# Optimization experiments

Hardware: AMD Instinct MI355X
Metric: run time of the kernel (lower is better)

## Reference

```python
import jax, jax.numpy as jnp
import numpy as np

N_DATASETS = 2
DATASET_CATS = (1536, 1536)
TOTAL_CATS = 3072
MAX_UNIFY = 1536
N_NODES = TOTAL_CATS + MAX_UNIFY  # 4608
LRELU_ALPHA = 0.2
BI_TEMP = 0.05
NEG_INF = -9e15


def setup_inputs() -> dict:
    key = jax.random.key(0)
    ks = jax.random.split(key, 12)
    nfeat, nfeat_out, nfeat_adj, nhid, nheads = 512, 256, 64, 64, 4
    att_out, mlp = 256, 512
    s = lambda k, sh: (jax.random.normal(k, sh, jnp.float32) * 0.05)
    return {
        'x': jax.random.normal(ks[0], (N_NODES, nfeat), jnp.float32),
        'W_before': s(ks[1], (nfeat, nfeat_out)),
        'b_before': jnp.zeros((nfeat_out,), jnp.float32),
        'W_adj': s(ks[2], (nfeat_out, nfeat_adj)),
        'b_adj': jnp.zeros((nfeat_adj,), jnp.float32),
        'W_heads': s(ks[3], (nheads, nfeat_out, nhid)),
        'a_heads': s(ks[4], (nheads, 2 * nhid)),
        'W_out': s(ks[5], (nheads * nhid, att_out)),
        'a_out': s(ks[6], (2 * att_out,)),
        'W_lin1': s(ks[7], (att_out, mlp)),
        'b_lin1': jnp.zeros((mlp,), jnp.float32),
    }


def _calc_adjacency(x_out, W_adj, b_adj):
    # linear_adj + L2 normalize + cosine similarity + row normalization via diag(1/rowsum)
    af = x_out @ W_adj + b_adj                              # [N, nfeat_adj]
    nrm = jnp.sqrt(jnp.sum(af * af, axis=1, keepdims=True))
    naf = af / jnp.maximum(nrm, 1e-12)
    sim = naf @ naf.T                                       # [N, N]
    rowsum = jnp.sum(sim, axis=1)
    r_inv = 1.0 / rowsum
    r_inv = jnp.where(jnp.isinf(r_inv), 0.0, r_inv)
    return r_inv[:, None] * sim                             # diag(1/rowsum) @ sim


def _gat_multihead(x, adj, W, a):
    # W: [H, F, d], a: [H, 2d]. Standard pyGAT dense attention, vectorized over heads.
    d = W.shape[-1]
    Wh = jnp.einsum('nf,hfd->hnd', x, W)                    # [H, N, d]
    f1 = jnp.einsum('hnd,hd->hn', Wh, a[:, :d])             # [H, N]
    f2 = jnp.einsum('hnd,hd->hn', Wh, a[:, d:])             # [H, N]
    e = jax.nn.leaky_relu(f1[:, :, None] + f2[:, None, :], LRELU_ALPHA)  # [H, N, N]
    att = jnp.where(adj[None] > 0, e, NEG_INF)
    att = jax.nn.softmax(att, axis=-1)
    return jnp.einsum('hnm,hmd->hnd', att, Wh)              # [H, N, d]


def _gat_single(x, adj, W, a):
    d = W.shape[-1]
    Wh = x @ W                                              # [N, d]
    f1 = Wh @ a[:d]
    f2 = Wh @ a[d:]
    e = jax.nn.leaky_relu(f1[:, None] + f2[None, :], LRELU_ALPHA)
    att = jnp.where(adj > 0, e, NEG_INF)
    att = jax.nn.softmax(att, axis=-1)
    return att @ Wh


def reference(x, W_before, b_before, W_adj, b_adj, W_heads, a_heads, W_out, a_out, W_lin1, b_lin1):
    x1 = x @ W_before + b_before                            # linear_before
    adj = _calc_adjacency(x1, W_adj, b_adj)                 # before relu, as in source
    x1 = jax.nn.relu(x1)
    # multi-head GAT layer 1 (concat=True -> elu per head, concat along feature dim)
    h = jax.nn.elu(_gat_multihead(x1, adj, W_heads, a_heads))   # [H, N, d]
    H, N, d = h.shape
    feat = jnp.transpose(h, (1, 0, 2)).reshape(N, H * d)
    x2 = feat + x1                                          # residual; dropout is eval no-op
    # output attention head (concat=False -> no elu inside)
    x3 = jax.nn.elu(_gat_single(x2, adj, W_out, a_out) + x2)
    feat_mlp = x3 @ W_lin1 + b_lin1                          # linear1
    # sep_bipartite_graphs: per-dataset column-softmax over unify columns
    bgs = []
    cur = 0
    for nc in DATASET_CATS:
        blk = adj[cur:cur + nc, TOTAL_CATS:]                 # [nc, MAX_UNIFY]
        bgs.append(jax.nn.softmax(blk / BI_TEMP, axis=0))
        cur += nc
    return (feat_mlp[TOTAL_CATS:],) + tuple(bgs)


if __name__ == '__main__':
    out = reference(**setup_inputs())
    for o in out:
        print(o.shape, o.dtype)
```

## Files before the change

### kernel.cpp

```cpp
#include <hip/hip_runtime.h>
#include <hip/hip_bf16.h>
#include <math.h>

constexpr int NTOT = 4608;
constexpr int TC   = 3072;
constexpr int MU   = 1536;
constexpr int NH   = 4;

constexpr long OFF_ADJ  = 0;
constexpr long OFF_X1   = OFF_ADJ  + (long)NTOT*NTOT;
constexpr long OFF_NAF  = OFF_X1   + (long)NTOT*256;
constexpr long OFF_PART = OFF_NAF  + (long)NTOT*64;
constexpr long OFF_RINV = OFF_PART + 72*64;
constexpr long OFF_WH   = OFF_RINV + NTOT;
constexpr long OFF_F1H  = OFF_WH   + (long)4*NTOT*64;
constexpr long OFF_F2H  = OFF_F1H  + (long)4*NTOT;
constexpr long OFF_MXH  = OFF_F2H  + (long)4*NTOT;
constexpr long OFF_CIH  = OFF_MXH  + (long)4*NTOT;
constexpr long OFF_X2   = OFF_CIH  + (long)4*NTOT;
constexpr long OFF_WH2  = OFF_X2   + (long)NTOT*256;
constexpr long OFF_F1S  = OFF_WH2  + (long)NTOT*256;
constexpr long OFF_F2S  = OFF_F1S  + NTOT;
constexpr long OFF_MXS  = OFF_F2S  + NTOT;
constexpr long OFF_CIS  = OFF_MXS  + NTOT;
constexpr long OFF_X3   = OFF_CIS  + NTOT;
constexpr long OFF_PMAX = OFF_X3   + (long)MU*256;
constexpr long OFF_PSUM = OFF_PMAX + (long)2*12*MU;
constexpr long OFF_FMAX = OFF_PSUM + (long)2*12*MU;
constexpr long OFF_FIS  = OFF_FMAX + (long)2*MU;
constexpr long OFF_L1   = OFF_FIS  + (long)2*MU;
constexpr long OFF_L2   = OFF_L1   + (long)4*NTOT;

typedef __attribute__((ext_vector_type(8))) short bf16x8;
typedef __attribute__((ext_vector_type(8))) unsigned short ushort8;
typedef __attribute__((ext_vector_type(4))) float floatx4;

__device__ __forceinline__ float lrelu(float x) { return (x >= 0.f) ? x : 0.2f * x; }
__device__ __forceinline__ float elu(float x)   { return (x > 0.f) ? x : expm1f(x); }
__device__ __forceinline__ unsigned short f2bf(float f) {
    unsigned u = __float_as_uint(f);
    u += 0x7FFFu + ((u >> 16) & 1u);
    return (unsigned short)(u >> 16);
}

__global__ __launch_bounds__(256) void zero_k(float* __restrict__ p)
{
    long idx = ((long)blockIdx.x * 256 + threadIdx.x) * 4;
    *(float4*)(p + idx) = make_float4(0.f, 0.f, 0.f, 0.f);
}

__global__ __launch_bounds__(256) void cvt_t(
    const float* __restrict__ in, unsigned short* __restrict__ out,
    int D, long inZ, long outZ)
{
    __shared__ float t[64][65];
    int n0 = blockIdx.x * 64, d0 = blockIdx.y * 64;
    const float* inz = in + (long)blockIdx.z * inZ;
    unsigned short* outz = out + (long)blockIdx.z * outZ;
    int tid = threadIdx.x;
    int r4 = tid >> 6, k = tid & 63;
    #pragma unroll
    for (int l = 0; l < 16; ++l) {
        int row = l * 4 + r4;
        t[row][k] = inz[(long)(n0 + row) * D + d0 + k];
    }
    __syncthreads();
    #pragma unroll
    for (int l = 0; l < 16; ++l) {
        int drow = l * 4 + r4;
        outz[(long)(d0 + drow) * NTOT + n0 + k] = f2bf(t[k][drow]);
    }
}

template<bool RELU_A, bool BIAS>
__global__ __launch_bounds__(256) void gemm_rm(
    const float* __restrict__ A, const float* __restrict__ B,
    const float* __restrict__ bias, float* __restrict__ C,
    int K, int M, long strideBz, long strideCz)
{
    __shared__ float As[16][68];
    __shared__ float Bs[16][68];
    const float* Bz = B + (long)blockIdx.z * strideBz;
    float* Cz = C + (long)blockIdx.z * strideCz;
    int tid = threadIdx.x;
    int r0 = blockIdx.x * 64;
    int c0 = blockIdx.y * 64;
    int ty = tid >> 4, tx = tid & 15;
    float acc[4][4] = {};
    for (int k0 = 0; k0 < K; k0 += 16) {
        #pragma unroll
        for (int l = 0; l < 4; ++l) {
            int idx = l * 256 + tid;
            int row = idx >> 4, kk = idx & 15;
            float v = A[(long)(r0 + row) * K + k0 + kk];
            if (RELU_A) v = fmaxf(v, 0.f);
            As[kk][row] = v;
        }
        #pragma unroll
        for (int l = 0; l < 4; ++l) {
            int idx = l * 256 + tid;
            int kk = idx >> 6, col = idx & 63;
            Bs[kk][col] = Bz[(long)(k0 + kk) * M + c0 + col];
        }
        __syncthreads();
        #pragma unroll
        for (int kk = 0; kk < 16; ++kk) {
            float av[4], bv[4];
            #pragma unroll
            for (int i = 0; i < 4; ++i) av[i] = As[kk][ty * 4 + i];
            #pragma unroll
            for (int j = 0; j < 4; ++j) bv[j] = Bs[kk][tx * 4 + j];
            #pragma unroll
            for (int i = 0; i < 4; ++i)
                #pragma unroll
                for (int j = 0; j < 4; ++j) acc[i][j] += av[i] * bv[j];
        }
        __syncthreads();
    }
    #pragma unroll
    for (int i = 0; i < 4; ++i) {
        int r = r0 + ty * 4 + i;
        #pragma unroll
        for (int j = 0; j < 4; ++j) {
            int c = c0 + tx * 4 + j;
            float v = acc[i][j];
            if (BIAS) v += bias[c];
            Cz[(long)r * M + c] = v;
        }
    }
}

__global__ __launch_bounds__(256) void af_naf(
    const float* __restrict__ x1, const float* __restrict__ W_adj,
    const float* __restrict__ b_adj, float* __restrict__ naf)
{
    __shared__ float rowbuf[4][256];
    int tid = threadIdx.x, w = tid >> 6, lane = tid & 63;
    int n = blockIdx.x * 4 + w;
    #pragma unroll
    for (int l = 0; l < 4; ++l) rowbuf[w][l * 64 + lane] = x1[(long)n * 256 + l * 64 + lane];
    __syncthreads();
    float acc = b_adj[lane];
    for (int k = 0; k < 256; ++k) acc += rowbuf[w][k] * W_adj[k * 64 + lane];
    float sq = acc * acc;
    #pragma unroll
    for (int off = 32; off >= 1; off >>= 1) sq += __shfl_xor(sq, off);
    float nrm = fmaxf(sqrtf(sq), 1e-12f);
    naf[(long)n * 64 + lane] = acc / nrm;
}

__global__ __launch_bounds__(256) void sim_k(
    const float* __restrict__ naf, float* __restrict__ sim)
{
    __shared__ float As[64][68];
    __shared__ float Bs[64][68];
    int tid = threadIdx.x;
    int n0 = blockIdx.x * 64, m0 = blockIdx.y * 64;
    int row4 = tid >> 6, k = tid & 63;
    #pragma unroll
    for (int l = 0; l < 16; ++l) {
        int row = l * 4 + row4;
        As[k][row] = naf[(long)(n0 + row) * 64 + k];
        Bs[k][row] = naf[(long)(m0 + row) * 64 + k];
    }
    __syncthreads();
    int ty = tid >> 4, tx = tid & 15;
    float acc[4][4] = {};
    for (int kk = 0; kk < 64; ++kk) {
        float4 av = *(const float4*)&As[kk][ty * 4];
        float4 bv = *(const float4*)&Bs[kk][tx * 4];
        float a[4] = { av.x, av.y, av.z, av.w };
        float b[4] = { bv.x, bv.y, bv.z, bv.w };
        #pragma unroll
        for (int i = 0; i < 4; ++i)
            #pragma unroll
            for (int j = 0; j < 4; ++j) acc[i][j] += a[i] * b[j];
    }
    #pragma unroll
    for (int i = 0; i < 4; ++i) {
        long r = n0 + ty * 4 + i;
        float4 o = make_float4(acc[i][0], acc[i][1], acc[i][2], acc[i][3]);
        *(float4*)(sim + r * NTOT + m0 + tx * 4) = o;
    }
}

__global__ __launch_bounds__(256) void rowsum_rinv_mask(
    const float* __restrict__ sim, float* __restrict__ rinv,
    unsigned long long* __restrict__ maskb)
{
    int tid = threadIdx.x, w = tid >> 6, lane = tid & 63;
    int n = blockIdx.x * 4 + w;
    const float* row = sim + (long)n * NTOT;
    double s = 0.0;
    for (int i = 0; i < 72; ++i) s += (double)row[i * 64 + lane];
    #pragma unroll
    for (int off = 32; off >= 1; off >>= 1) s += __shfl_xor(s, off);
    float rs = (float)s;
    float r = 1.0f / rs;
    if (isinf(r)) r = 0.f;
    if (lane == 0) rinv[n] = r;
    for (int i = 0; i < 72; ++i) {
        float v = row[i * 64 + lane];
        unsigned long long wball = __ballot((v * r) > 0.0f);
        if (lane == 0) maskb[(long)n * 72 + i] = wball;
    }
}

__global__ __launch_bounds__(256) void dots_k(
    const float* __restrict__ Wh, const float* __restrict__ a,
    float* __restrict__ f1, float* __restrict__ f2, int D)
{
    int tid = threadIdx.x, w = tid >> 6, lane = tid & 63;
    int n = blockIdx.x * 4 + w;
    int h = blockIdx.y;
    const float* row = Wh + ((long)h * NTOT + n) * D;
    const float* a1 = a + (long)h * 2 * D;
    const float* a2 = a1 + D;
    float p1 = 0.f, p2 = 0.f;
    for (int d = lane; d < D; d += 64) {
        float v = row[d];
        p1 += v * a1[d];
        p2 += v * a2[d];
    }
    #pragma unroll
    for (int off = 32; off >= 1; off >>= 1) { p1 += __shfl_xor(p1, off); p2 += __shfl_xor(p2, off); }
    if (lane == 0) { f1[(long)h * NTOT + n] = p1; f2[(long)h * NTOT + n] = p2; }
}

__global__ __launch_bounds__(256) void mh_attn(
    const unsigned long long* __restrict__ maskb,
    const float* __restrict__ f1, const float* __restrict__ f2,
    const unsigned short* __restrict__ Whbf, float* __restrict__ accb,
    float* __restrict__ lbuf)
{
    __shared__ unsigned short Ws[2][64][72];
    int tid = threadIdx.x;
    int wave = tid >> 6, lane = tid & 63;
    int n0 = blockIdx.x * 64;
    int h = blockIdx.y, ch = blockIdx.z;
    const float* f2h = f2 + (long)h * NTOT;
    const unsigned short* Wb = Whbf + (long)h * 64 * NTOT;
    int wd = tid >> 2, wc = (tid & 3) * 16;
    int arow = lane & 15, acol8 = (lane >> 4) * 8;
    int n = n0 + 16 * wave + arow;
    float r1 = f1[(long)h * NTOT + n];
    float lsum = 0.f;
    floatx4 acc[4] = {};
    int buf = 0;
    for (int mt = ch * 12; mt < ch * 12 + 12; ++mt) {
        int m0 = mt * 64;
        ushort8 wv0 = *(const ushort8*)&Wb[(long)wd * NTOT + m0 + wc];
        ushort8 wv1 = *(const ushort8*)&Wb[(long)wd * NTOT + m0 + wc + 8];
        unsigned long long mw = maskb[(long)n * 72 + mt];
        bf16x8 afr[2];
        #pragma unroll
        for (int ks = 0; ks < 2; ++ks) {
            int mc = m0 + ks * 32 + acol8;
            float4 fv0 = *(const float4*)(f2h + mc);
            float4 fv1 = *(const float4*)(f2h + mc + 4);
            unsigned bits = (unsigned)(mw >> (ks * 32 + acol8)) & 0xFFu;
            float f[8] = { fv0.x, fv0.y, fv0.z, fv0.w, fv1.x, fv1.y, fv1.z, fv1.w };
            #pragma unroll
            for (int j = 0; j < 8; ++j) {
                float s = r1 + f[j];
                float e = __expf(fmaxf(s, 0.2f * s));
                float p = ((bits >> j) & 1u) ? e : 0.f;
                lsum += p;
                afr[ks][j] = (short)f2bf(p);
            }
        }
        *(ushort8*)&Ws[buf][wd][wc] = wv0;
        *(ushort8*)&Ws[buf][wd][wc + 8] = wv1;
        __syncthreads();
        #pragma unroll
        for (int ks = 0; ks < 2; ++ks) {
            #pragma unroll
            for (int dt = 0; dt < 4; ++dt) {
                bf16x8 bfr = *(bf16x8*)&Ws[buf][16 * dt + arow][ks * 32 + acol8];
                acc[dt] = __builtin_amdgcn_mfma_f32_16x16x32_bf16(afr[ks], bfr, acc[dt], 0, 0, 0);
            }
        }
        buf ^= 1;
    }
    lsum += __shfl_xor(lsum, 16);
    lsum += __shfl_xor(lsum, 32);
    if (lane < 16) atomicAdd(lbuf + (long)h * NTOT + n0 + 16 * wave + lane, lsum);
    int crow = n0 + 16 * wave + (lane >> 4) * 4;
    int ccol = h * 64 + (lane & 15);
    #pragma unroll
    for (int dt = 0; dt < 4; ++dt)
        #pragma unroll
        for (int r = 0; r < 4; ++r)
            atomicAdd(accb + (long)(crow + r) * 256 + ccol + dt * 16, acc[dt][r]);
}

__global__ __launch_bounds__(256) void mh_fin(
    const float* __restrict__ accb, const float* __restrict__ lbuf,
    const float* __restrict__ x1, float* __restrict__ x2)
{
    long idx = ((long)blockIdx.x * 256 + threadIdx.x) * 4;
    long r = idx >> 8;
    int h = (int)((idx & 255) >> 6);
    float l = lbuf[(long)h * NTOT + r];
    float inv = (l > 0.f) ? 1.0f / l : 0.f;
    float4 a = *(const float4*)(accb + idx);
    float4 xv = *(const float4*)(x1 + idx);
    float4 o;
    o.x = elu(a.x * inv) + fmaxf(xv.x, 0.f);
    o.y = elu(a.y * inv) + fmaxf(xv.y, 0.f);
    o.z = elu(a.z * inv) + fmaxf(xv.z, 0.f);
    o.w = elu(a.w * inv) + fmaxf(xv.w, 0.f);
    *(float4*)(x2 + idx) = o;
}

__global__ __launch_bounds__(256) void s_attn(
    const unsigned long long* __restrict__ maskb,
    const float* __restrict__ f1, const float* __restrict__ f2,
    const unsigned short* __restrict__ Wh2bf, float* __restrict__ accb,
    float* __restrict__ lbuf)
{
    __shared__ unsigned short Ws[2][64][72];
    int tid = threadIdx.x;
    int wave = tid >> 6, lane = tid & 63;
    int lr0 = blockIdx.x * 32;
    int c0 = blockIdx.y * 64;
    int ch = blockIdx.z;
    int wd = tid >> 2, wc = (tid & 3) * 16;
    int arow = lane & 15, acol8 = (lane >> 4) * 8;
    int rt = wave & 1;
    int dt0 = (wave >> 1) * 2;
    int n = TC + lr0 + 16 * rt + arow;
    float r1 = f1[n];
    float lsum = 0.f;
    floatx4 acc[2] = {};
    int buf = 0;
    for (int mt = ch * 12; mt < ch * 12 + 12; ++mt) {
        int m0 = mt * 64;
        ushort8 wv0 = *(const ushort8*)&Wh2bf[(long)(c0 + wd) * NTOT + m0 + wc];
        ushort8 wv1 = *(const ushort8*)&Wh2bf[(long)(c0 + wd) * NTOT + m0 + wc + 8];
        unsigned long long mw = maskb[(long)n * 72 + mt];
        bf16x8 afr[2];
        #pragma unroll
        for (int ks = 0; ks < 2; ++ks) {
            int mc = m0 + ks * 32 + acol8;
            float4 fv0 = *(const float4*)(f2 + mc);
            float4 fv1 = *(const float4*)(f2 + mc + 4);
            unsigned bits = (unsigned)(mw >> (ks * 32 + acol8)) & 0xFFu;
            float f[8] = { fv0.x, fv0.y, fv0.z, fv0.w, fv1.x, fv1.y, fv1.z, fv1.w };
            #pragma unroll
            for (int j = 0; j < 8; ++j) {
                float s = r1 + f[j];
                float e = __expf(fmaxf(s, 0.2f * s));
                float p = ((bits >> j) & 1u) ? e : 0.f;
                lsum += p;
                afr[ks][j] = (short)f2bf(p);
            }
        }
        *(ushort8*)&Ws[buf][wd][wc] = wv0;
        *(ushort8*)&Ws[buf][wd][wc + 8] = wv1;
        __syncthreads();
        #pragma unroll
        for (int ks = 0; ks < 2; ++ks) {
            #pragma unroll
            for (int t = 0; t < 2; ++t) {
                bf16x8 bfr = *(bf16x8*)&Ws[buf][16 * (dt0 + t) + arow][ks * 32 + acol8];
                acc[t] = __builtin_amdgcn_mfma_f32_16x16x32_bf16(afr[ks], bfr, acc[t], 0, 0, 0);
            }
        }
        buf ^= 1;
    }
    lsum += __shfl_xor(lsum, 16);
    lsum += __shfl_xor(lsum, 32);
    if (blockIdx.y == 0 && wave < 2 && lane < 16)
        atomicAdd(lbuf + lr0 + 16 * wave + lane, lsum);
    int crow = lr0 + 16 * rt + (lane >> 4) * 4;
    int ccol = c0 + (lane & 15);
    #pragma unroll
    for (int t = 0; t < 2; ++t)
        #pragma unroll
        for (int r = 0; r < 4; ++r)
            atomicAdd(accb + (long)(crow + r) * 256 + ccol + (dt0 + t) * 16, acc[t][r]);
}

__global__ __launch_bounds__(256) void s_fin(
    const float* __restrict__ accb, const float* __restrict__ lbuf,
    const float* __restrict__ x2, float* __restrict__ x3)
{
    long idx = ((long)blockIdx.x * 256 + threadIdx.x) * 4;
    long r = idx >> 8;
    float l = lbuf[r];
    float inv = (l > 0.f) ? 1.0f / l : 0.f;
    float4 a = *(const float4*)(accb + idx);
    float4 xv = *(const float4*)(x2 + (long)TC * 256 + idx);
    float4 o;
    o.x = elu(a.x * inv + xv.x);
    o.y = elu(a.y * inv + xv.y);
    o.z = elu(a.z * inv + xv.z);
    o.w = elu(a.w * inv + xv.w);
    *(float4*)(x3 + idx) = o;
}

__global__ __launch_bounds__(256) void bi_partial(
    const float* __restrict__ sim, const float* __restrict__ rinv,
    float* __restrict__ pmax, float* __restrict__ psum)
{
    int c = blockIdx.x * 256 + threadIdx.x;
    int ch = blockIdx.y;
    int ds = blockIdx.z;
    float m = -3.0e38f, s = 0.f;
    int rbase = ds * MU + ch * 128;
    for (int r = 0; r < 128; ++r) {
        float a = sim[(long)(rbase + r) * NTOT + TC + c] * rinv[rbase + r];
        float v = a * 20.0f;
        if (v <= m) s += expf(v - m);
        else { s = s * expf(m - v) + 1.f; m = v; }
    }
    pmax[((long)ds * 12 + ch) * MU + c] = m;
    psum[((long)ds * 12 + ch) * MU + c] = s;
}

__global__ __launch_bounds__(256) void bi_combine(
    const float* __restrict__ pmax, const float* __restrict__ psum,
    float* __restrict__ fmax, float* __restrict__ fis)
{
    int b = blockIdx.x;
    int ds = b / 6, ct = b % 6;
    int c = ct * 256 + threadIdx.x;
    float m = -3.0e38f;
    for (int ch = 0; ch < 12; ++ch) m = fmaxf(m, pmax[((long)ds * 12 + ch) * MU + c]);
    float s = 0.f;
    for (int ch = 0; ch < 12; ++ch)
        s += psum[((long)ds * 12 + ch) * MU + c] * expf(pmax[((long)ds * 12 + ch) * MU + c] - m);
    fmax[ds * MU + c] = m;
    fis[ds * MU + c] = 1.0f / s;
}

__global__ __launch_bounds__(256) void bi_norm(
    const float* __restrict__ sim, const float* __restrict__ rinv,
    const float* __restrict__ fmax, const float* __restrict__ fis,
    float* __restrict__ outbg)
{
    int c = blockIdx.x * 256 + threadIdx.x;
    int ch = blockIdx.y;
    int ds = blockIdx.z;
    float m = fmax[ds * MU + c], inv = fis[ds * MU + c];
    long obase = (long)ds * MU * MU;
    int rbase = ch * 128;
    for (int r = 0; r < 128; ++r) {
        int row = ds * MU + rbase + r;
        float a = sim[(long)row * NTOT + TC + c] * rinv[row];
        float v = a * 20.0f;
        outbg[obase + (long)(rbase + r) * MU + c] = expf(v - m) * inv;
    }
}

extern "C" void kernel_launch(void* const* d_in, const int* in_sizes, int n_in,
                              void* d_out, int out_size, void* d_ws, size_t ws_size,
                              hipStream_t stream)
{
    const float* x        = (const float*)d_in[0];
    const float* W_before = (const float*)d_in[1];
    const float* b_before = (const float*)d_in[2];
    const float* W_adj    = (const float*)d_in[3];
    const float* b_adj    = (const float*)d_in[4];
    const float* W_heads  = (const float*)d_in[5];
    const float* a_heads  = (const float*)d_in[6];
    const float* W_out    = (const float*)d_in[7];
    const float* a_out    = (const float*)d_in[8];
    const float* W_lin1   = (const float*)d_in[9];
    const float* b_lin1   = (const float*)d_in[10];
    float* out = (float*)d_out;
    float* ws  = (float*)d_ws;

    float* sim  = ws + OFF_ADJ;
    float* x1p  = ws + OFF_X1;
    float* naf  = ws + OFF_NAF;
    float* rinv = ws + OFF_RINV;
    float* Wh   = ws + OFF_WH;
    float* f1h  = ws + OFF_F1H;
    float* f2h  = ws + OFF_F2H;
    float* x2   = ws + OFF_X2;
    float* Wh2  = ws + OFF_WH2;
    float* f1s  = ws + OFF_F1S;
    float* f2s  = ws + OFF_F2S;
    float* x3   = ws + OFF_X3;
    float* pmax = ws + OFF_PMAX;
    float* psum = ws + OFF_PSUM;
    float* fmx  = ws + OFF_FMAX;
    float* fis  = ws + OFF_FIS;
    float* l1   = ws + OFF_L1;
    float* l2   = ws + OFF_L2;
    float* acc1 = ws + OFF_WH2;
    float* acc2 = ws + OFF_X1;
    unsigned short* Whbf  = (unsigned short*)(ws + OFF_X2);
    unsigned short* Wh2bf = (unsigned short*)(ws + OFF_X1 + (long)MU * 256);
    unsigned long long* maskb = (unsigned long long*)(ws + OFF_WH);

    dim3 b256(256);

    zero_k<<<dim3(NTOT * 256 / 1024), b256, 0, stream>>>(acc1);
    zero_k<<<dim3(20), b256, 0, stream>>>(l1);
    gemm_rm<false, true><<<dim3(72, 4, 1), b256, 0, stream>>>(x, W_before, b_before, x1p, 512, 256, 0, 0);
    af_naf<<<dim3(1152), b256, 0, stream>>>(x1p, W_adj, b_adj, naf);
    sim_k<<<dim3(72, 72), b256, 0, stream>>>(naf, sim);
    gemm_rm<true, false><<<dim3(72, 1, 4), b256, 0, stream>>>(x1p, W_heads, nullptr, Wh, 256, 64,
                                                              (long)256 * 64, (long)NTOT * 64);
    cvt_t<<<dim3(72, 1, 4), b256, 0, stream>>>(Wh, Whbf, 64, (long)NTOT * 64, (long)64 * NTOT);
    dots_k<<<dim3(1152, 4), b256, 0, stream>>>(Wh, a_heads, f1h, f2h, 64);
    rowsum_rinv_mask<<<dim3(1152), b256, 0, stream>>>(sim, rinv, maskb);
    mh_attn<<<dim3(72, 4, 6), b256, 0, stream>>>(maskb, f1h, f2h, Whbf, acc1, l1);
    mh_fin<<<dim3(NTOT * 256 / 1024), b256, 0, stream>>>(acc1, l1, x1p, x2);
    zero_k<<<dim3(MU * 256 / 1024), b256, 0, stream>>>(acc2);
    gemm_rm<false, false><<<dim3(72, 4, 1), b256, 0, stream>>>(x2, W_out, nullptr, Wh2, 256, 256, 0, 0);
    cvt_t<<<dim3(72, 4, 1), b256, 0, stream>>>(Wh2, Wh2bf, 256, 0, 0);
    dots_k<<<dim3(1152, 1), b256, 0, stream>>>(Wh2, a_out, f1s, f2s, 256);
    s_attn<<<dim3(48, 4, 6), b256, 0, stream>>>(maskb, f1s, f2s, Wh2bf, acc2, l2);
    s_fin<<<dim3(MU * 256 / 1024), b256, 0, stream>>>(acc2, l2, x2, x3);
    gemm_rm<false, true><<<dim3(24, 8, 1), b256, 0, stream>>>(x3, W_lin1, b_lin1, out, 256, 512, 0, 0);
    bi_partial<<<dim3(6, 12, 2), b256, 0, stream>>>(sim, rinv, pmax, psum);
    bi_combine<<<dim3(12), b256, 0, stream>>>(pmax, psum, fmx, fis);
    bi_norm<<<dim3(6, 12, 2), b256, 0, stream>>>(sim, rinv, fmx, fis, out + (long)MU * 512);
}
```

Before: 429.0 us.

## Fuse row sums and sign masks into similarity kernel, store only needed block

The similarity kernel now computes per-tile double row partial sums and positive-sign bitmasks in its epilogue. It writes the full similarity values only for the category-by-unify block that the bipartite softmax needs. A small finalize kernel combines the partials into rinv and derives the adjacency mask by flipping the bits when rinv is negative. This removes the write and reread of the full 4608x4608 float matrix, at the cost of extra shuffles, shared-memory staging and two small workspace arrays in the sim epilogue.

```diff
diff --git a/kernel.cpp b/kernel.cpp
--- a/kernel.cpp
+++ b/kernel.cpp
@@ -30,6 +30,8 @@
 constexpr long OFF_FIS  = OFF_FMAX + (long)2*MU;
 constexpr long OFF_L1   = OFF_FIS  + (long)2*MU;
 constexpr long OFF_L2   = OFF_L1   + (long)4*NTOT;
+constexpr long OFF_PARTS = OFF_ADJ + (long)TC*NTOT;
+constexpr long OFF_POSB  = OFF_PARTS + 2L*NTOT*72;
 
 typedef __attribute__((ext_vector_type(8))) short bf16x8;
 typedef __attribute__((ext_vector_type(8))) unsigned short ushort8;
@@ -150,10 +152,12 @@
 }
 
 __global__ __launch_bounds__(256) void sim_k(
-    const float* __restrict__ naf, float* __restrict__ sim)
+    const float* __restrict__ naf, float* __restrict__ sim,
+    double* __restrict__ parts, unsigned long long* __restrict__ posb)
 {
     __shared__ float As[64][68];
     __shared__ float Bs[64][68];
+    __shared__ unsigned char sgn[64][16];
     int tid = threadIdx.x;
     int n0 = blockIdx.x * 64, m0 = blockIdx.y * 64;
     int row4 = tid >> 6, k = tid & 63;
@@ -176,33 +180,58 @@
             #pragma unroll
             for (int j = 0; j < 4; ++j) acc[i][j] += a[i] * b[j];
     }
+    if (m0 >= TC && n0 < TC) {
+        #pragma unroll
+        for (int i = 0; i < 4; ++i) {
+            long r = n0 + ty * 4 + i;
+            float4 o = make_float4(acc[i][0], acc[i][1], acc[i][2], acc[i][3]);
+            *(float4*)(sim + r * NTOT + m0 + tx * 4) = o;
+        }
+    }
+    int mt = m0 >> 6;
     #pragma unroll
     for (int i = 0; i < 4; ++i) {
-        long r = n0 + ty * 4 + i;
-        float4 o = make_float4(acc[i][0], acc[i][1], acc[i][2], acc[i][3]);
-        *(float4*)(sim + r * NTOT + m0 + tx * 4) = o;
-    }
-}
-
-__global__ __launch_bounds__(256) void rowsum_rinv_mask(
-    const float* __restrict__ sim, float* __restrict__ rinv,
-    unsigned long long* __restrict__ maskb)
+        double t = (double)acc[i][0] + (double)acc[i][1] + (double)acc[i][2] + (double)acc[i][3];
+        #pragma unroll
+        for (int off = 1; off < 16; off <<= 1) t += __shfl_xor(t, off);
+        unsigned nib = (unsigned)(acc[i][0] > 0.f) | ((unsigned)(acc[i][1] > 0.f) << 1)
+                     | ((unsigned)(acc[i][2] > 0.f) << 2) | ((unsigned)(acc[i][3] > 0.f) << 3);
+        sgn[ty * 4 + i][tx] = (unsigned char)nib;
+        if (tx == 0) parts[(long)(n0 + ty * 4 + i) * 72 + mt] = t;
+    }
+    __syncthreads();
+    if (tid < 64) {
+        unsigned long long w = 0;
+        #pragma unroll
+        for (int t = 0; t < 16; ++t)
+            w |= (unsigned long long)sgn[tid][t] << (4 * t);
+        posb[(long)(n0 + tid) * 72 + mt] = w;
+    }
+}
+
+__global__ __launch_bounds__(256) void rowfin(
+    const double* __restrict__ parts, const unsigned long long* __restrict__ posb,
+    float* __restrict__ rinv, unsigned long long* __restrict__ maskb)
 {
     int tid = threadIdx.x, w = tid >> 6, lane = tid & 63;
     int n = blockIdx.x * 4 + w;
-    const float* row = sim + (long)n * NTOT;
-    double s = 0.0;
-    for (int i = 0; i < 72; ++i) s += (double)row[i * 64 + lane];
+    double s = parts[(long)n * 72 + lane];
+    if (lane < 8) s += parts[(long)n * 72 + 64 + lane];
     #pragma unroll
     for (int off = 32; off >= 1; off >>= 1) s += __shfl_xor(s, off);
     float rs = (float)s;
     float r = 1.0f / rs;
     if (isinf(r)) r = 0.f;
     if (lane == 0) rinv[n] = r;
-    for (int i = 0; i < 72; ++i) {
-        float v = row[i * 64 + lane];
-        unsigned long long wball = __ballot((v * r) > 0.0f);
-        if (lane == 0) maskb[(long)n * 72 + i] = wball;
+    unsigned long long pw = posb[(long)n * 72 + lane];
+    unsigned long long mw = (r < 0.f) ? ~pw : pw;
+    if (r == 0.f) mw = 0ull;
+    maskb[(long)n * 72 + lane] = mw;
+    if (lane < 8) {
+        pw = posb[(long)n * 72 + 64 + lane];
+        mw = (r < 0.f) ? ~pw : pw;
+        if (r == 0.f) mw = 0ull;
+        maskb[(long)n * 72 + 64 + lane] = mw;
     }
 }
 
@@ -495,6 +524,8 @@
     unsigned short* Whbf  = (unsigned short*)(ws + OFF_X2);
     unsigned short* Wh2bf = (unsigned short*)(ws + OFF_X1 + (long)MU * 256);
     unsigned long long* maskb = (unsigned long long*)(ws + OFF_WH);
+    double* parts = (double*)(ws + OFF_PARTS);
+    unsigned long long* posb = (unsigned long long*)(ws + OFF_POSB);
 
     dim3 b256(256);
 
@@ -502,12 +533,12 @@
     zero_k<<<dim3(20), b256, 0, stream>>>(l1);
     gemm_rm<false, true><<<dim3(72, 4, 1), b256, 0, stream>>>(x, W_before, b_before, x1p, 512, 256, 0, 0);
     af_naf<<<dim3(1152), b256, 0, stream>>>(x1p, W_adj, b_adj, naf);
-    sim_k<<<dim3(72, 72), b256, 0, stream>>>(naf, sim);
+    sim_k<<<dim3(72, 72), b256, 0, stream>>>(naf, sim, parts, posb);
     gemm_rm<true, false><<<dim3(72, 1, 4), b256, 0, stream>>>(x1p, W_heads, nullptr, Wh, 256, 64,
                                                               (long)256 * 64, (long)NTOT * 64);
     cvt_t<<<dim3(72, 1, 4), b256, 0, stream>>>(Wh, Whbf, 64, (long)NTOT * 64, (long)64 * NTOT);
     dots_k<<<dim3(1152, 4), b256, 0, stream>>>(Wh, a_heads, f1h, f2h, 64);
-    rowsum_rinv_mask<<<dim3(1152), b256, 0, stream>>>(sim, rinv, maskb);
+    rowfin<<<dim3(1152), b256, 0, stream>>>(parts, posb, rinv, maskb);
     mh_attn<<<dim3(72, 4, 6), b256, 0, stream>>>(maskb, f1h, f2h, Whbf, acc1, l1);
     mh_fin<<<dim3(NTOT * 256 / 1024), b256, 0, stream>>>(acc1, l1, x1p, x2);
     zero_k<<<dim3(MU * 256 / 1024), b256, 0, stream>>>(acc2);
```

After: 401.3 us. -6.5%, faster.
